# Performance work log

Hardware: AMD Instinct MI355X
Metric: run time of the kernel (lower is better)

## Reference

```python
import jax, jax.numpy as jnp
import numpy as np

ED = 1024   # encoder_dim
GH = 1024   # gnn_hidden
NL = 3      # gnn_layers
NH = 8      # gnn_heads
HD = GH // NH
N = 2048    # graph nodes
B = 1024    # query/doc batch
TEMP = 0.05
LAPW = 0.1

def _layernorm(x, g, b):
    mu = jnp.mean(x, axis=-1, keepdims=True)
    var = jnp.mean((x - mu) ** 2, axis=-1, keepdims=True)
    return (x - mu) * jax.lax.rsqrt(var + 1e-5) * g + b

def _mlp_proj(x, W1, b1, g, beta, W2, b2):
    h = _layernorm(x @ W1 + b1, g, beta)
    h = jax.nn.gelu(h, approximate=False)
    return h @ W2 + b2

def _l2norm(x):
    n = jnp.linalg.norm(x, axis=-1, keepdims=True)
    return x / jnp.maximum(n, 1e-12)

def _gnn(x, adj, gatW, a1, a2, ln_g, ln_b, poW, pob):
    mask = adj > 0
    for l in range(NL):
        Wh = jnp.einsum('nf,hfo->hno', x, gatW[l])            # [H,N,HD]
        # a([Wh_i, Wh_j]) == Wh_i@a1 + Wh_j@a2 (linear, no bias): avoids NxNx2F concat
        s1 = jnp.einsum('hno,ho->hn', Wh, a1[l])
        s2 = jnp.einsum('hno,ho->hn', Wh, a2[l])
        e = jax.nn.leaky_relu(s1[:, :, None] + s2[:, None, :], 0.2)  # [H,N,N]
        att = jax.nn.softmax(jnp.where(mask[None], e, -9e15), axis=-1)
        h = jnp.einsum('hnm,hmo->hno', att, Wh)               # [H,N,HD]
        h = jnp.transpose(h, (1, 0, 2)).reshape(x.shape[0], GH)  # concat heads
        h = jax.nn.elu(_layernorm(h, ln_g[l], ln_b[l]))
        x = x + h  # in_features == hidden so residual applies every layer
    return x @ poW + pob

def _forward(query_embeds, pos_doc_embeds, node_embeds, adj, laplacian, params):
    (qW1, qb1, qg, qbt, qW2, qb2,
     dW1, db1, dg, dbt, dW2, db2,
     gatW, a1, a2, ln_g, ln_b, poW, pob) = params
    graph_embeds = _gnn(node_embeds, adj, gatW, a1, a2, ln_g, ln_b, poW, pob)
    q = _l2norm(_mlp_proj(query_embeds, qW1, qb1, qg, qbt, qW2, qb2))
    p = _l2norm(_mlp_proj(pos_doc_embeds, dW1, db1, dg, dbt, dW2, db2))
    pos_sim = jnp.sum(q * p, axis=-1) / TEMP                  # [B]
    neg_sim = (q @ p.T) / TEMP                                # [B,B]
    logits = jnp.concatenate([pos_sim[:, None], neg_sim], axis=1)
    info_nce = jnp.mean(jax.nn.logsumexp(logits, axis=-1) - logits[:, 0])
    lap = jnp.sum(graph_embeds * (laplacian @ graph_embeds)) / graph_embeds.shape[0]
    return info_nce + LAPW * lap, info_nce, lap

def setup_inputs() -> dict:
    key = jax.random.key(0)
    ks = jax.random.split(key, 24)
    r = lambda k, s: jax.random.normal(k, s, jnp.float32) * 0.02
    adj = (jax.random.uniform(ks[3], (N, N)) < 0.02).astype(jnp.float32)
    adj = jnp.maximum(adj, jnp.eye(N, dtype=jnp.float32))
    return {
        'query_embeds': jax.random.normal(ks[0], (B, ED), jnp.float32),
        'pos_doc_embeds': jax.random.normal(ks[1], (B, ED), jnp.float32),
        'node_embeds': jax.random.normal(ks[2], (N, ED), jnp.float32),
        'adj': adj,
        'laplacian': r(ks[4], (N, N)),
        'qW1': r(ks[5], (ED, ED)), 'qb1': jnp.zeros((ED,), jnp.float32),
        'qg': jnp.ones((ED,), jnp.float32), 'qbt': jnp.zeros((ED,), jnp.float32),
        'qW2': r(ks[6], (ED, ED)), 'qb2': jnp.zeros((ED,), jnp.float32),
        'dW1': r(ks[7], (ED, ED)), 'db1': jnp.zeros((ED,), jnp.float32),
        'dg': jnp.ones((ED,), jnp.float32), 'dbt': jnp.zeros((ED,), jnp.float32),
        'dW2': r(ks[8], (ED, ED)), 'db2': jnp.zeros((ED,), jnp.float32),
        'gatW': r(ks[9], (NL, NH, ED, HD)),
        'a1': r(ks[10], (NL, NH, HD)),
        'a2': r(ks[11], (NL, NH, HD)),
        'ln_g': jnp.ones((NL, GH), jnp.float32),
        'ln_b': jnp.zeros((NL, GH), jnp.float32),
        'poW': r(ks[12], (GH, ED)),
        'pob': jnp.zeros((ED,), jnp.float32),
    }

def reference(query_embeds, pos_doc_embeds, node_embeds, adj, laplacian,
              qW1, qb1, qg, qbt, qW2, qb2,
              dW1, db1, dg, dbt, dW2, db2,
              gatW, a1, a2, ln_g, ln_b, poW, pob):
    params = (qW1, qb1, qg, qbt, qW2, qb2,
              dW1, db1, dg, dbt, dW2, db2,
              gatW, a1, a2, ln_g, ln_b, poW, pob)
    return _forward(query_embeds, pos_doc_embeds, node_embeds, adj, laplacian, params)
```

## Files before the change

### kernel.cpp

```cpp
#include <hip/hip_runtime.h>
#include <math.h>

#define ED    1024
#define GH    1024
#define NLAY  3
#define NHEAD 8
#define HD    128
#define NNODE 2048
#define BQ    1024
#define CAP   192
#define CAPP  208

typedef unsigned short u16;
typedef __attribute__((ext_vector_type(8))) short short8;
typedef __attribute__((ext_vector_type(4))) float f32x4;

static const size_t OFF_X    = 0;
static const size_t OFF_XB   = 2097152;
static const size_t OFF_WHB  = 3145728;
static const size_t OFF_WTG  = 4194304;
static const size_t OFF_WTPO = 5767168;
static const size_t OFF_WTQ1 = 6291456;
static const size_t OFF_WTD1 = 6815744;
static const size_t OFF_WTQ2 = 7340032;
static const size_t OFF_WTD2 = 7864320;
static const size_t OFF_G    = 8388608;
static const size_t OFF_GT   = 10485760;
static const size_t OFF_QPB  = 11534336;
static const size_t OFF_HF   = 12582912;
static const size_t OFF_HB   = 14680064;
static const size_t OFF_FF   = 15728640;
static const size_t OFF_FB   = 17825792;
static const size_t OFF_NEG  = 18874368;
static const size_t OFF_SV1  = 19922944;
static const size_t OFF_SV2  = 19939328;
static const size_t OFF_ACC  = 19955712;
static const size_t OFF_CNT  = 19955714;
static const size_t OFF_NCNT = 19955720;
static const size_t OFF_NBR  = 19957768;

__device__ __forceinline__ u16 f2bf(float f) {
  unsigned int u = __float_as_uint(f);
  return (u16)((u + 0x7fffu + ((u >> 16) & 1u)) >> 16);
}
__device__ __forceinline__ float bf2f(u16 u) {
  return __uint_as_float(((unsigned int)u) << 16);
}

__device__ __forceinline__ float waveSum(float v) {
#pragma unroll
  for (int off = 32; off; off >>= 1) v += __shfl_xor(v, off, 64);
  return v;
}
__device__ __forceinline__ float waveMax(float v) {
#pragma unroll
  for (int off = 32; off; off >>= 1) v = fmaxf(v, __shfl_xor(v, off, 64));
  return v;
}
__device__ __forceinline__ float blockSum(float v) {
  __shared__ float buf[4];
  int lane = threadIdx.x & 63, wid = threadIdx.x >> 6, nw = (blockDim.x + 63) >> 6;
  v = waveSum(v);
  __syncthreads();
  if (lane == 0) buf[wid] = v;
  __syncthreads();
  float r = buf[0];
  for (int i = 1; i < nw; ++i) r += buf[i];
  return r;
}
__device__ __forceinline__ float blockMax(float v) {
  __shared__ float buf[4];
  int lane = threadIdx.x & 63, wid = threadIdx.x >> 6, nw = (blockDim.x + 63) >> 6;
  v = waveMax(v);
  __syncthreads();
  if (lane == 0) buf[wid] = v;
  __syncthreads();
  float r = buf[0];
  for (int i = 1; i < nw; ++i) r = fmaxf(r, buf[i]);
  return r;
}

__global__ __launch_bounds__(256) void gemm128(
    const u16* __restrict__ A, const u16* __restrict__ B0,
    const u16* __restrict__ B1, float* __restrict__ C, u16* __restrict__ Cb,
    u16* __restrict__ Ct,
    const float* __restrict__ bias0, const float* __restrict__ bias1,
    int M, int N, int K, int split, float scale) {
  __shared__ u16 As[2][128][32];
  __shared__ u16 Bs[2][128][32];
  const int tid = threadIdx.x, wave = tid >> 6, lane = tid & 63;
  const int bm = blockIdx.y * 128, bn = blockIdx.x * 128;
  const u16* Bt = (bm < split) ? B0 : B1;
  const float* bias = (bm < split) ? bias0 : bias1;

  const int sr = tid >> 2, ss = tid & 3;
  const u16* ga0 = A  + (size_t)(bm + sr) * K + ss * 8;
  const u16* ga1 = A  + (size_t)(bm + sr + 64) * K + ss * 8;
  const u16* gb0 = Bt + (size_t)(bn + sr) * K + ss * 8;
  const u16* gb1 = Bt + (size_t)(bn + sr + 64) * K + ss * 8;

  const int r16 = lane & 15, kg = lane >> 4;
  const int wm = (wave >> 1) * 64, wn = (wave & 1) * 64;

  f32x4 acc[4][4] = {};
  const int nk = K >> 5;

  float4 pa0 = *(const float4*)ga0;
  float4 pa1 = *(const float4*)ga1;
  float4 pb0 = *(const float4*)gb0;
  float4 pb1 = *(const float4*)gb1;

  for (int kt = 0; kt < nk; ++kt) {
    const int p = kt & 1;
    *(float4*)&As[p][sr][ss * 8]      = pa0;
    *(float4*)&As[p][sr + 64][ss * 8] = pa1;
    *(float4*)&Bs[p][sr][ss * 8]      = pb0;
    *(float4*)&Bs[p][sr + 64][ss * 8] = pb1;
    __syncthreads();
    if (kt + 1 < nk) {
      ga0 += 32; ga1 += 32; gb0 += 32; gb1 += 32;
      pa0 = *(const float4*)ga0;
      pa1 = *(const float4*)ga1;
      pb0 = *(const float4*)gb0;
      pb1 = *(const float4*)gb1;
    }
    short8 av[4], bv[4];
#pragma unroll
    for (int i = 0; i < 4; ++i)
      av[i] = *(const short8*)&As[p][wm + i * 16 + r16][kg * 8];
#pragma unroll
    for (int j = 0; j < 4; ++j)
      bv[j] = *(const short8*)&Bs[p][wn + j * 16 + r16][kg * 8];
#pragma unroll
    for (int i = 0; i < 4; ++i)
#pragma unroll
      for (int j = 0; j < 4; ++j)
        acc[i][j] = __builtin_amdgcn_mfma_f32_16x16x32_bf16(av[i], bv[j], acc[i][j], 0, 0, 0);
  }

  if (C) {
#pragma unroll
    for (int j = 0; j < 4; ++j) {
      int col = bn + wn + j * 16 + r16;
      float bvv = bias ? bias[col] : 0.f;
#pragma unroll
      for (int i = 0; i < 4; ++i) {
        int row0 = bm + wm + i * 16 + kg * 4;
        float* cp = C + (size_t)row0 * N + col;
#pragma unroll
        for (int r = 0; r < 4; ++r)
          cp[(size_t)r * N] = acc[i][j][r] * scale + bvv;
      }
    }
  }
  if (Cb) {
#pragma unroll
    for (int j = 0; j < 4; ++j) {
      int col = bn + wn + j * 16 + r16;
      float bvv = bias ? bias[col] : 0.f;
#pragma unroll
      for (int i = 0; i < 4; ++i) {
        int row0 = bm + wm + i * 16 + kg * 4;
        u16* cp = Cb + (size_t)row0 * N + col;
#pragma unroll
        for (int r = 0; r < 4; ++r)
          cp[(size_t)r * N] = f2bf(acc[i][j][r] * scale + bvv);
      }
    }
  }
  if (Ct) {
#pragma unroll
    for (int j = 0; j < 4; ++j) {
      int col = bn + wn + j * 16 + r16;
      float bvv = bias ? bias[col] : 0.f;
#pragma unroll
      for (int i = 0; i < 4; ++i) {
        int row0 = bm + wm + i * 16 + kg * 4;
        ushort4 o;
        o.x = f2bf(acc[i][j][0] * scale + bvv);
        o.y = f2bf(acc[i][j][1] * scale + bvv);
        o.z = f2bf(acc[i][j][2] * scale + bvv);
        o.w = f2bf(acc[i][j][3] * scale + bvv);
        *(ushort4*)&Ct[(size_t)col * M + row0] = o;
      }
    }
  }
}

__global__ __launch_bounds__(256) void gemm_dual(
    const u16* __restrict__ A0, const u16* __restrict__ B00,
    const u16* __restrict__ B01, float* __restrict__ C0, u16* __restrict__ D0,
    const float* __restrict__ e0, const float* __restrict__ f0, int M0, int sp0, float sc0,
    const float* __restrict__ A1v, const float* __restrict__ A2v,
    float* __restrict__ S1o, float* __restrict__ S2o,
    const u16* __restrict__ A1, const u16* __restrict__ B10,
    const u16* __restrict__ B11, float* __restrict__ C1, u16* __restrict__ D1,
    const float* __restrict__ e1, const float* __restrict__ f1, int M1, int sp1, float sc1) {
  const int z = blockIdx.z;
  const u16* A   = z ? A1 : A0;
  const u16* Bt0 = z ? B10 : B00;
  const u16* Bt1 = z ? B11 : B01;
  float* C = z ? C1 : C0;
  u16*   D = z ? D1 : D0;
  const float* bias0 = z ? e1 : e0;
  const float* bias1 = z ? f1 : f0;
  const int M = z ? M1 : M0, split = z ? sp1 : sp0;
  const float scale = z ? sc1 : sc0;
  const int bm = blockIdx.y * 128, bn = blockIdx.x * 128;
  if (bm >= M) return;
  const int N = 1024, K = 1024;
  const u16* Bt = (bm < split) ? Bt0 : Bt1;
  const float* bias = (bm < split) ? bias0 : bias1;

  __shared__ u16 As[2][128][32];
  __shared__ u16 Bs[2][128][32];
  const int tid = threadIdx.x, wave = tid >> 6, lane = tid & 63;
  const int sr = tid >> 2, ss = tid & 3;
  const u16* ga0 = A  + (size_t)(bm + sr) * K + ss * 8;
  const u16* ga1 = A  + (size_t)(bm + sr + 64) * K + ss * 8;
  const u16* gb0 = Bt + (size_t)(bn + sr) * K + ss * 8;
  const u16* gb1 = Bt + (size_t)(bn + sr + 64) * K + ss * 8;
  const int r16 = lane & 15, kg = lane >> 4;
  const int wm = (wave >> 1) * 64, wn = (wave & 1) * 64;

  f32x4 acc[4][4] = {};
  const int nk = 32;

  float4 pa0 = *(const float4*)ga0;
  float4 pa1 = *(const float4*)ga1;
  float4 pb0 = *(const float4*)gb0;
  float4 pb1 = *(const float4*)gb1;

  for (int kt = 0; kt < nk; ++kt) {
    const int p = kt & 1;
    *(float4*)&As[p][sr][ss * 8]      = pa0;
    *(float4*)&As[p][sr + 64][ss * 8] = pa1;
    *(float4*)&Bs[p][sr][ss * 8]      = pb0;
    *(float4*)&Bs[p][sr + 64][ss * 8] = pb1;
    __syncthreads();
    if (kt + 1 < nk) {
      ga0 += 32; ga1 += 32; gb0 += 32; gb1 += 32;
      pa0 = *(const float4*)ga0;
      pa1 = *(const float4*)ga1;
      pb0 = *(const float4*)gb0;
      pb1 = *(const float4*)gb1;
    }
    short8 av[4], bv[4];
#pragma unroll
    for (int i = 0; i < 4; ++i)
      av[i] = *(const short8*)&As[p][wm + i * 16 + r16][kg * 8];
#pragma unroll
    for (int j = 0; j < 4; ++j)
      bv[j] = *(const short8*)&Bs[p][wn + j * 16 + r16][kg * 8];
#pragma unroll
    for (int i = 0; i < 4; ++i)
#pragma unroll
      for (int j = 0; j < 4; ++j)
        acc[i][j] = __builtin_amdgcn_mfma_f32_16x16x32_bf16(av[i], bv[j], acc[i][j], 0, 0, 0);
  }

  if (C) {
#pragma unroll
    for (int j = 0; j < 4; ++j) {
      int col = bn + wn + j * 16 + r16;
      float bvv = bias ? bias[col] : 0.f;
#pragma unroll
      for (int i = 0; i < 4; ++i) {
        int row0 = bm + wm + i * 16 + kg * 4;
        float* cp = C + (size_t)row0 * N + col;
#pragma unroll
        for (int r = 0; r < 4; ++r)
          cp[(size_t)r * N] = acc[i][j][r] * scale + bvv;
      }
    }
  }
  if (D) {
#pragma unroll
    for (int j = 0; j < 4; ++j) {
      int col = bn + wn + j * 16 + r16;
      float bvv = bias ? bias[col] : 0.f;
#pragma unroll
      for (int i = 0; i < 4; ++i) {
        int row0 = bm + wm + i * 16 + kg * 4;
        u16* cp = D + (size_t)row0 * N + col;
#pragma unroll
        for (int r = 0; r < 4; ++r)
          cp[(size_t)r * N] = f2bf(acc[i][j][r] * scale + bvv);
      }
    }
  }

  if (z == 0 && S1o) {
    float c1[4], c2[4];
#pragma unroll
    for (int j = 0; j < 4; ++j) {
      int col = bn + wn + j * 16 + r16;
      c1[j] = A1v[col]; c2[j] = A2v[col];
    }
    float r1[4][4], r2[4][4];
#pragma unroll
    for (int i = 0; i < 4; ++i)
#pragma unroll
      for (int r = 0; r < 4; ++r) {
        float v1 = 0.f, v2 = 0.f;
#pragma unroll
        for (int j = 0; j < 4; ++j) {
          v1 += acc[i][j][r] * c1[j];
          v2 += acc[i][j][r] * c2[j];
        }
#pragma unroll
        for (int off = 8; off; off >>= 1) {
          v1 += __shfl_xor(v1, off, 64);
          v2 += __shfl_xor(v2, off, 64);
        }
        r1[i][r] = v1; r2[i][r] = v2;
      }
    __syncthreads();
    float* sb1 = (float*)&As[0][0][0];
    float* sb2 = sb1 + 256;
    if (r16 == 0) {
      int half = wn >> 6;
#pragma unroll
      for (int i = 0; i < 4; ++i)
#pragma unroll
        for (int r = 0; r < 4; ++r) {
          int row = wm + i * 16 + kg * 4 + r;
          sb1[half * 128 + row] = r1[i][r];
          sb2[half * 128 + row] = r2[i][r];
        }
    }
    __syncthreads();
    if (tid < 128) {
      int h = blockIdx.x;
      S1o[(h << 11) + bm + tid] = sb1[tid] + sb1[128 + tid];
      S2o[(h << 11) + bm + tid] = sb2[tid] + sb2[128 + tid];
    }
  }
}

__global__ __launch_bounds__(256) void lap_gemm(
    const float* __restrict__ A, const u16* __restrict__ Bt,
    const float* __restrict__ G, float* __restrict__ acc,
    int* __restrict__ cnt_done, float* __restrict__ out) {
  __shared__ u16 As[2][128][32];
  __shared__ u16 Bs[2][128][32];
  const int tid = threadIdx.x, wave = tid >> 6, lane = tid & 63;
  const int n = blockIdx.x;
  const int bn = (n >> 7) * 128, strip = n & 127;
  const int bm = (strip & 15) * 128, k0 = (strip >> 4) * 256;

  const int sr = tid >> 2, ss = tid & 3;
  const float* gA0 = A + (size_t)(bm + sr) * NNODE + k0 + ss * 8;
  const float* gA1 = gA0 + (size_t)64 * NNODE;
  const u16* gb0 = Bt + (size_t)(bn + sr) * NNODE + k0 + ss * 8;
  const u16* gb1 = Bt + (size_t)(bn + sr + 64) * NNODE + k0 + ss * 8;

  const int r16 = lane & 15, kg = lane >> 4;
  const int wm = (wave >> 1) * 64, wn = (wave & 1) * 64;

  f32x4 acc_r[4][4] = {};
  const int nk = 8;

  float4 a0l = *(const float4*)gA0, a0h = *(const float4*)(gA0 + 4);
  float4 a1l = *(const float4*)gA1, a1h = *(const float4*)(gA1 + 4);
  float4 pb0 = *(const float4*)gb0;
  float4 pb1 = *(const float4*)gb1;

  for (int kt = 0; kt < nk; ++kt) {
    const int p = kt & 1;
    {
      union { short8 v; ushort4 u4[2]; } w;
      w.u4[0].x = f2bf(a0l.x); w.u4[0].y = f2bf(a0l.y);
      w.u4[0].z = f2bf(a0l.z); w.u4[0].w = f2bf(a0l.w);
      w.u4[1].x = f2bf(a0h.x); w.u4[1].y = f2bf(a0h.y);
      w.u4[1].z = f2bf(a0h.z); w.u4[1].w = f2bf(a0h.w);
      *(short8*)&As[p][sr][ss * 8] = w.v;
      w.u4[0].x = f2bf(a1l.x); w.u4[0].y = f2bf(a1l.y);
      w.u4[0].z = f2bf(a1l.z); w.u4[0].w = f2bf(a1l.w);
      w.u4[1].x = f2bf(a1h.x); w.u4[1].y = f2bf(a1h.y);
      w.u4[1].z = f2bf(a1h.z); w.u4[1].w = f2bf(a1h.w);
      *(short8*)&As[p][sr + 64][ss * 8] = w.v;
    }
    *(float4*)&Bs[p][sr][ss * 8]      = pb0;
    *(float4*)&Bs[p][sr + 64][ss * 8] = pb1;
    __syncthreads();
    if (kt + 1 < nk) {
      gA0 += 32; gA1 += 32; gb0 += 32; gb1 += 32;
      a0l = *(const float4*)gA0; a0h = *(const float4*)(gA0 + 4);
      a1l = *(const float4*)gA1; a1h = *(const float4*)(gA1 + 4);
      pb0 = *(const float4*)gb0;
      pb1 = *(const float4*)gb1;
    }
    short8 av[4], bv[4];
#pragma unroll
    for (int i = 0; i < 4; ++i)
      av[i] = *(const short8*)&As[p][wm + i * 16 + r16][kg * 8];
#pragma unroll
    for (int j = 0; j < 4; ++j)
      bv[j] = *(const short8*)&Bs[p][wn + j * 16 + r16][kg * 8];
#pragma unroll
    for (int i = 0; i < 4; ++i)
#pragma unroll
      for (int j = 0; j < 4; ++j)
        acc_r[i][j] = __builtin_amdgcn_mfma_f32_16x16x32_bf16(av[i], bv[j], acc_r[i][j], 0, 0, 0);
  }

  float sum = 0.f;
#pragma unroll
  for (int j = 0; j < 4; ++j) {
    int col = bn + wn + j * 16 + r16;
#pragma unroll
    for (int i = 0; i < 4; ++i) {
      int row0 = bm + wm + i * 16 + kg * 4;
      const float* gp = G + (size_t)row0 * ED + col;
#pragma unroll
      for (int r = 0; r < 4; ++r)
        sum += acc_r[i][j][r] * gp[(size_t)r * ED];
    }
  }
  sum = blockSum(sum);
  if (tid == 0) {
    atomicAdd(acc, sum);
    __threadfence();
    int prev = atomicAdd(cnt_done, 1);
    if (prev == (int)gridDim.x - 1) {
      float lap  = atomicAdd(acc, 0.f) / 2048.f;
      float info = atomicAdd(acc + 1, 0.f) / 1024.f;
      out[0] = info + 0.1f * lap;
      out[1] = info;
      out[2] = lap;
    }
  }
}

__global__ __launch_bounds__(256) void att_elem(
    const u16* __restrict__ WHb, const float* __restrict__ S1,
    const float* __restrict__ S2, const int* __restrict__ nbr,
    const int* __restrict__ ncnt, float* __restrict__ X, u16* __restrict__ Xb,
    const float* __restrict__ g, const float* __restrict__ b,
    int mode, const float* __restrict__ EIN, u16* __restrict__ EOUT,
    const float* __restrict__ g0, const float* __restrict__ b0,
    const float* __restrict__ g1, const float* __restrict__ b1,
    float* __restrict__ acc) {
  const int t = threadIdx.x;
  if (blockIdx.x < NNODE) {
    __shared__ int snb[CAPP];
    __shared__ float pw[NHEAD][CAPP];
    const int n = blockIdx.x;
    const int h = t >> 5, l = t & 31;
    const int cnt = ncnt[n];
    const int cntP = (cnt + 15) & ~15;
    for (int j = t; j < cnt; j += 256) snb[j] = nbr[n * CAP + j];
    __syncthreads();
    for (int j = cnt + t; j < cntP; j += 256) snb[j] = snb[0];

    const float s1v = S1[(h << 11) + n];
    float ev[6];
    float lmax = -1e30f;
    int ne = 0;
    for (int j = l; j < cnt; j += 32) {
      float e = s1v + S2[(h << 11) + snb[j]];
      e = e > 0.f ? e : 0.2f * e;
      ev[ne++] = e;
      lmax = fmaxf(lmax, e);
    }
#pragma unroll
    for (int off = 16; off; off >>= 1) lmax = fmaxf(lmax, __shfl_xor(lmax, off, 64));
    float lsum = 0.f;
    ne = 0;
    for (int j = l; j < cnt; j += 32) {
      float p = __expf(ev[ne++] - lmax);
      pw[h][j] = p;
      lsum += p;
    }
    for (int j = cnt + l; j < cntP; j += 32) pw[h][j] = 0.f;
#pragma unroll
    for (int off = 16; off; off >>= 1) lsum += __shfl_xor(lsum, off, 64);
    const float inv = 1.f / lsum;
    __syncthreads();

    float o0 = 0.f, o1 = 0.f, o2 = 0.f, o3 = 0.f;
    const u16* wp = WHb + (t << 2);
    for (int j0 = 0; j0 < cntP; j0 += 16) {
      ushort4 buf[16];
#pragma unroll
      for (int u = 0; u < 16; ++u)
        buf[u] = *(const ushort4*)(wp + ((size_t)snb[j0 + u] << 10));
#pragma unroll
      for (int u = 0; u < 16; ++u) {
        float w = pw[h][j0 + u];
        o0 += w * bf2f(buf[u].x);
        o1 += w * bf2f(buf[u].y);
        o2 += w * bf2f(buf[u].z);
        o3 += w * bf2f(buf[u].w);
      }
    }
    o0 *= inv; o1 *= inv; o2 *= inv; o3 *= inv;

    float s  = o0 + o1 + o2 + o3;
    float sq = o0 * o0 + o1 * o1 + o2 * o2 + o3 * o3;
    float mean = blockSum(s) * (1.f / 1024.f);
    float var  = blockSum(sq) * (1.f / 1024.f) - mean * mean;
    float rstd = rsqrtf(fmaxf(var, 0.f) + 1e-5f);
    float4 xv = *(float4*)&X[((size_t)n << 10) + (t << 2)];
    float ov[4] = {o0, o1, o2, o3};
    float xa[4] = {xv.x, xv.y, xv.z, xv.w};
#pragma unroll
    for (int i = 0; i < 4; ++i) {
      int c = (t << 2) + i;
      float y = (ov[i] - mean) * rstd * g[c] + b[c];
      y = y > 0.f ? y : expm1f(y);
      xa[i] += y;
    }
    *(float4*)&X[((size_t)n << 10) + (t << 2)] = make_float4(xa[0], xa[1], xa[2], xa[3]);
    ushort4 o;
    o.x = f2bf(xa[0]); o.y = f2bf(xa[1]); o.z = f2bf(xa[2]); o.w = f2bf(xa[3]);
    *(ushort4*)&Xb[((size_t)n << 10) + (t << 2)] = o;
  } else {
    const int row = blockIdx.x - NNODE;
    if (mode == 0) {
      const float* gg = (row < 1024) ? g0 : g1;
      const float* bb = (row < 1024) ? b0 : b1;
      float4 v = *(const float4*)&EIN[((size_t)row << 10) + (t << 2)];
      float s = v.x + v.y + v.z + v.w;
      float sq = v.x * v.x + v.y * v.y + v.z * v.z + v.w * v.w;
      float mean = blockSum(s) * (1.f / 1024.f);
      float var = blockSum(sq) * (1.f / 1024.f) - mean * mean;
      float rstd = rsqrtf(fmaxf(var, 0.f) + 1e-5f);
      float vals[4] = {v.x, v.y, v.z, v.w};
      ushort4 o;
      u16* oa = (u16*)&o;
#pragma unroll
      for (int i = 0; i < 4; ++i) {
        int c = (t << 2) + i;
        float y = (vals[i] - mean) * rstd * gg[c] + bb[c];
        y = 0.5f * y * (1.f + erff(y * 0.70710678118654752f));
        oa[i] = f2bf(y);
      }
      *(ushort4*)&EOUT[((size_t)row << 10) + (t << 2)] = o;
    } else if (mode == 1) {
      float4 v = *(const float4*)&EIN[((size_t)row << 10) + (t << 2)];
      float sq = v.x * v.x + v.y * v.y + v.z * v.z + v.w * v.w;
      float s = blockSum(sq);
      float inv = 1.f / fmaxf(sqrtf(s), 1e-12f);
      ushort4 o;
      o.x = f2bf(v.x * inv); o.y = f2bf(v.y * inv);
      o.z = f2bf(v.z * inv); o.w = f2bf(v.w * inv);
      *(ushort4*)&EOUT[((size_t)row << 10) + (t << 2)] = o;
    } else {
      const float* rw = EIN + ((size_t)row << 10);
      float4 v = *(const float4*)&rw[t << 2];
      float lm = fmaxf(fmaxf(v.x, v.y), fmaxf(v.z, v.w));
      float m = blockMax(lm);
      float ls = __expf(v.x - m) + __expf(v.y - m) + __expf(v.z - m) + __expf(v.w - m);
      float ssum = blockSum(ls);
      if (t == 0) {
        float pos = rw[row];
        float loss = m + logf(ssum + __expf(pos - m)) - pos;
        atomicAdd(acc + 1, loss);
      }
    }
  }
}

__global__ __launch_bounds__(256) void prep_mega(
    const float* __restrict__ adj, int* __restrict__ nbr, int* __restrict__ ncnt,
    float* __restrict__ acc, int* __restrict__ cnt_done,
    const float* __restrict__ nodes, float* __restrict__ Xf, u16* __restrict__ Xb,
    const float* __restrict__ q, const float* __restrict__ d, u16* __restrict__ QPb) {
  const int bx = blockIdx.x, tid = threadIdx.x;
  if (bx < NNODE) {
    __shared__ int cnt;
    if (bx == 0 && tid < 2) acc[tid] = 0.f;
    if (bx == 0 && tid == 2) *cnt_done = 0;
    if (tid == 0) cnt = 0;
    __syncthreads();
    for (int c = tid; c < NNODE; c += 256) {
      if (adj[((size_t)bx << 11) + c] > 0.f) {
        int p = atomicAdd(&cnt, 1);
        if (p < CAP) nbr[bx * CAP + p] = c;
      }
    }
    __syncthreads();
    if (tid == 0) ncnt[bx] = cnt < CAP ? cnt : CAP;
  } else if (bx < 2 * NNODE) {
    int i = (bx - NNODE) * 256 + tid;
    float4 v = ((const float4*)nodes)[i];
    ((float4*)Xf)[i] = v;
    ushort4 o;
    o.x = f2bf(v.x); o.y = f2bf(v.y); o.z = f2bf(v.z); o.w = f2bf(v.w);
    ((ushort4*)Xb)[i] = o;
  } else {
    int i = (bx - 2 * NNODE) * 256 + tid;
    const int half = BQ * ED / 4;
    const float* src = (i < half) ? q : d;
    int j = (i < half) ? i : i - half;
    float4 v = ((const float4*)src)[j];
    ushort4 o;
    o.x = f2bf(v.x); o.y = f2bf(v.y); o.z = f2bf(v.z); o.w = f2bf(v.w);
    ((ushort4*)QPb)[i] = o;
  }
}

__device__ __forceinline__ void cvt_tr_body(const float* ip, u16* op, int R, int C) {
  __shared__ float T[64][65];
  int r0 = blockIdx.y * 64, c0 = blockIdx.x * 64;
  int t = threadIdx.x;
#pragma unroll
  for (int p = 0; p < 4; ++p) {
    int row = p * 16 + (t >> 4), col = (t & 15) * 4;
    float4 v = *(const float4*)&ip[(size_t)(r0 + row) * C + c0 + col];
    T[row][col] = v.x; T[row][col + 1] = v.y;
    T[row][col + 2] = v.z; T[row][col + 3] = v.w;
  }
  __syncthreads();
#pragma unroll
  for (int p = 0; p < 4; ++p) {
    int c = p * 16 + (t >> 4), r = (t & 15) * 4;
    ushort4 o;
    o.x = f2bf(T[r][c]); o.y = f2bf(T[r + 1][c]);
    o.z = f2bf(T[r + 2][c]); o.w = f2bf(T[r + 3][c]);
    *(ushort4*)&op[(size_t)(c0 + c) * R + r0 + r] = o;
  }
}

__global__ __launch_bounds__(256) void cvt_transpose(
    const float* __restrict__ in, u16* __restrict__ out,
    int R, int C, long inb, long outb) {
  cvt_tr_body(in + (size_t)blockIdx.z * inb, out + (size_t)blockIdx.z * outb, R, C);
}

__global__ __launch_bounds__(256) void cvt_transpose5(
    const float* __restrict__ i0, u16* __restrict__ o0,
    const float* __restrict__ i1, u16* __restrict__ o1,
    const float* __restrict__ i2, u16* __restrict__ o2,
    const float* __restrict__ i3, u16* __restrict__ o3,
    const float* __restrict__ i4, u16* __restrict__ o4) {
  const float* in; u16* out;
  switch (blockIdx.z) {
    case 0: in = i0; out = o0; break;
    case 1: in = i1; out = o1; break;
    case 2: in = i2; out = o2; break;
    case 3: in = i3; out = o3; break;
    default: in = i4; out = o4; break;
  }
  cvt_tr_body(in, out, 1024, 1024);
}

extern "C" void kernel_launch(void* const* d_in, const int* in_sizes, int n_in,
                              void* d_out, int out_size, void* d_ws, size_t ws_size,
                              hipStream_t stream) {
  const float* query = (const float*)d_in[0];
  const float* docs  = (const float*)d_in[1];
  const float* nodes = (const float*)d_in[2];
  const float* adj   = (const float*)d_in[3];
  const float* lapl  = (const float*)d_in[4];
  const float* qW1 = (const float*)d_in[5],  *qb1 = (const float*)d_in[6];
  const float* qg  = (const float*)d_in[7],  *qbt = (const float*)d_in[8];
  const float* qW2 = (const float*)d_in[9],  *qb2 = (const float*)d_in[10];
  const float* dW1 = (const float*)d_in[11], *db1 = (const float*)d_in[12];
  const float* dg  = (const float*)d_in[13], *dbt = (const float*)d_in[14];
  const float* dW2 = (const float*)d_in[15], *db2 = (const float*)d_in[16];
  const float* gatW = (const float*)d_in[17];
  const float* a1   = (const float*)d_in[18];
  const float* a2   = (const float*)d_in[19];
  const float* ln_g = (const float*)d_in[20];
  const float* ln_b = (const float*)d_in[21];
  const float* poW  = (const float*)d_in[22];
  const float* pob  = (const float*)d_in[23];
  float* out = (float*)d_out;

  float* ws = (float*)d_ws;
  float* X    = ws + OFF_X;
  u16*   Xb   = (u16*)(ws + OFF_XB);
  u16*   WHb  = (u16*)(ws + OFF_WHB);
  u16*   WtG  = (u16*)(ws + OFF_WTG);
  u16*   WtPO = (u16*)(ws + OFF_WTPO);
  u16*   WtQ1 = (u16*)(ws + OFF_WTQ1);
  u16*   WtD1 = (u16*)(ws + OFF_WTD1);
  u16*   WtQ2 = (u16*)(ws + OFF_WTQ2);
  u16*   WtD2 = (u16*)(ws + OFF_WTD2);
  float* G    = ws + OFF_G;
  u16*   Gt   = (u16*)(ws + OFF_GT);
  u16*   QPb  = (u16*)(ws + OFF_QPB);
  float* Hf   = ws + OFF_HF;
  u16*   Hb   = (u16*)(ws + OFF_HB);
  float* Ff   = ws + OFF_FF;
  u16*   Fb   = (u16*)(ws + OFF_FB);
  float* NEG  = ws + OFF_NEG;
  float* S1v  = ws + OFF_SV1;
  float* S2v  = ws + OFF_SV2;
  float* ACC  = ws + OFF_ACC;
  int*   CNTD = (int*)(ws + OFF_CNT);
  int*   NCNT = (int*)(ws + OFF_NCNT);
  int*   NBR  = (int*)(ws + OFF_NBR);

  const size_t WSL = (size_t)GH * ED;

  prep_mega<<<3 * NNODE, 256, 0, stream>>>(
      adj, NBR, NCNT, ACC, CNTD, nodes, X, Xb, query, docs, QPb);
  cvt_transpose<<<dim3(2, 16, 24), 256, 0, stream>>>(
      gatW, WtG, ED, HD, (long)ED * HD, (long)HD * ED);
  cvt_transpose5<<<dim3(16, 16, 5), 256, 0, stream>>>(
      poW, WtPO, qW1, WtQ1, dW1, WtD1, qW2, WtQ2, dW2, WtD2);

  gemm_dual<<<dim3(8, 16, 2), 256, 0, stream>>>(
      Xb, WtG, WtG, nullptr, WHb, nullptr, nullptr, NNODE, NNODE, 1.f,
      a1, a2, S1v, S2v,
      QPb, WtQ1, WtD1, Hf, nullptr, qb1, db1, 2 * BQ, BQ, 1.f);
  att_elem<<<NNODE + 2 * BQ, 256, 0, stream>>>(
      WHb, S1v, S2v, NBR, NCNT, X, Xb, ln_g, ln_b,
      0, Hf, Hb, qg, qbt, dg, dbt, ACC);

  gemm_dual<<<dim3(8, 16, 2), 256, 0, stream>>>(
      Xb, WtG + WSL, WtG + WSL, nullptr, WHb, nullptr, nullptr, NNODE, NNODE, 1.f,
      a1 + NHEAD * HD, a2 + NHEAD * HD, S1v, S2v,
      Hb, WtQ2, WtD2, Ff, nullptr, qb2, db2, 2 * BQ, BQ, 1.f);
  att_elem<<<NNODE + 2 * BQ, 256, 0, stream>>>(
      WHb, S1v, S2v, NBR, NCNT, X, Xb, ln_g + GH, ln_b + GH,
      1, Ff, Fb, nullptr, nullptr, nullptr, nullptr, ACC);

  gemm_dual<<<dim3(8, 16, 2), 256, 0, stream>>>(
      Xb, WtG + 2 * WSL, WtG + 2 * WSL, nullptr, WHb, nullptr, nullptr, NNODE, NNODE, 1.f,
      a1 + 2 * NHEAD * HD, a2 + 2 * NHEAD * HD, S1v, S2v,
      Fb, Fb + (size_t)BQ * ED, Fb + (size_t)BQ * ED, NEG, nullptr,
      nullptr, nullptr, BQ, BQ, 20.f);
  att_elem<<<NNODE + BQ, 256, 0, stream>>>(
      WHb, S1v, S2v, NBR, NCNT, X, Xb, ln_g + 2 * GH, ln_b + 2 * GH,
      2, NEG, nullptr, nullptr, nullptr, nullptr, nullptr, ACC);

  gemm128<<<dim3(ED / 128, NNODE / 128), 256, 0, stream>>>(
      Xb, WtPO, WtPO, G, nullptr, Gt, pob, pob, NNODE, ED, GH, NNODE, 1.f);
  lap_gemm<<<1024, 256, 0, stream>>>(lapl, Gt, G, ACC, CNTD, out);
}
```

Baseline: 386.2 us.

## Compute Laplacian term as <L, G·Gᵀ> and swizzle LDS tiles in GEMMs

The Laplacian penalty sum(G * (L @ G)) is now computed as the Frobenius dot of L with G·Gᵀ. The new kernel forms 128x128 tiles of G·Gᵀ from bf16 G with K=1024 and dots them with fp32 L tiles, instead of streaming L through a K=2048 GEMM and reading G in fp32. This drops the fp32 G and transposed G outputs and the per-element fp32-to-bf16 conversion of L. All GEMM kernels also get an XOR swizzle on their shared-memory tile layout to reduce LDS bank conflicts. The grid shrinks from 1024 to 256 blocks, which may lower occupancy, and G now enters the result only in bf16.

```diff
diff --git a/kernel.cpp b/kernel.cpp
--- a/kernel.cpp
+++ b/kernel.cpp
@@ -24,8 +24,7 @@
 static const size_t OFF_WTD1 = 6815744;
 static const size_t OFF_WTQ2 = 7340032;
 static const size_t OFF_WTD2 = 7864320;
-static const size_t OFF_G    = 8388608;
-static const size_t OFF_GT   = 10485760;
+static const size_t OFF_GB   = 8388608;
 static const size_t OFF_QPB  = 11534336;
 static const size_t OFF_HF   = 12582912;
 static const size_t OFF_HB   = 14680064;
@@ -80,10 +79,11 @@
   return r;
 }
 
+#define SWZ(row, seg) (((seg) ^ (((row) >> 1) & 3)) << 3)
+
 __global__ __launch_bounds__(256) void gemm128(
     const u16* __restrict__ A, const u16* __restrict__ B0,
     const u16* __restrict__ B1, float* __restrict__ C, u16* __restrict__ Cb,
-    u16* __restrict__ Ct,
     const float* __restrict__ bias0, const float* __restrict__ bias1,
     int M, int N, int K, int split, float scale) {
   __shared__ u16 As[2][128][32];
@@ -94,6 +94,7 @@
   const float* bias = (bm < split) ? bias0 : bias1;
 
   const int sr = tid >> 2, ss = tid & 3;
+  const int so = SWZ(sr, ss);
   const u16* ga0 = A  + (size_t)(bm + sr) * K + ss * 8;
   const u16* ga1 = A  + (size_t)(bm + sr + 64) * K + ss * 8;
   const u16* gb0 = Bt + (size_t)(bn + sr) * K + ss * 8;
@@ -112,10 +113,10 @@
 
   for (int kt = 0; kt < nk; ++kt) {
     const int p = kt & 1;
-    *(float4*)&As[p][sr][ss * 8]      = pa0;
-    *(float4*)&As[p][sr + 64][ss * 8] = pa1;
-    *(float4*)&Bs[p][sr][ss * 8]      = pb0;
-    *(float4*)&Bs[p][sr + 64][ss * 8] = pb1;
+    *(float4*)&As[p][sr][so]      = pa0;
+    *(float4*)&As[p][sr + 64][so] = pa1;
+    *(float4*)&Bs[p][sr][so]      = pb0;
+    *(float4*)&Bs[p][sr + 64][so] = pb1;
     __syncthreads();
     if (kt + 1 < nk) {
       ga0 += 32; ga1 += 32; gb0 += 32; gb1 += 32;
@@ -126,11 +127,15 @@
     }
     short8 av[4], bv[4];
 #pragma unroll
-    for (int i = 0; i < 4; ++i)
-      av[i] = *(const short8*)&As[p][wm + i * 16 + r16][kg * 8];
-#pragma unroll
-    for (int j = 0; j < 4; ++j)
-      bv[j] = *(const short8*)&Bs[p][wn + j * 16 + r16][kg * 8];
+    for (int i = 0; i < 4; ++i) {
+      int row = wm + i * 16 + r16;
+      av[i] = *(const short8*)&As[p][row][SWZ(row, kg)];
+    }
+#pragma unroll
+    for (int j = 0; j < 4; ++j) {
+      int col = wn + j * 16 + r16;
+      bv[j] = *(const short8*)&Bs[p][col][SWZ(col, kg)];
+    }
 #pragma unroll
     for (int i = 0; i < 4; ++i)
 #pragma unroll
@@ -165,23 +170,6 @@
 #pragma unroll
         for (int r = 0; r < 4; ++r)
           cp[(size_t)r * N] = f2bf(acc[i][j][r] * scale + bvv);
-      }
-    }
-  }
-  if (Ct) {
-#pragma unroll
-    for (int j = 0; j < 4; ++j) {
-      int col = bn + wn + j * 16 + r16;
-      float bvv = bias ? bias[col] : 0.f;
-#pragma unroll
-      for (int i = 0; i < 4; ++i) {
-        int row0 = bm + wm + i * 16 + kg * 4;
-        ushort4 o;
-        o.x = f2bf(acc[i][j][0] * scale + bvv);
-        o.y = f2bf(acc[i][j][1] * scale + bvv);
-        o.z = f2bf(acc[i][j][2] * scale + bvv);
-        o.w = f2bf(acc[i][j][3] * scale + bvv);
-        *(ushort4*)&Ct[(size_t)col * M + row0] = o;
       }
     }
   }
@@ -216,6 +204,7 @@
   __shared__ u16 Bs[2][128][32];
   const int tid = threadIdx.x, wave = tid >> 6, lane = tid & 63;
   const int sr = tid >> 2, ss = tid & 3;
+  const int so = SWZ(sr, ss);
   const u16* ga0 = A  + (size_t)(bm + sr) * K + ss * 8;
   const u16* ga1 = A  + (size_t)(bm + sr + 64) * K + ss * 8;
   const u16* gb0 = Bt + (size_t)(bn + sr) * K + ss * 8;
@@ -233,10 +222,10 @@
 
   for (int kt = 0; kt < nk; ++kt) {
     const int p = kt & 1;
-    *(float4*)&As[p][sr][ss * 8]      = pa0;
-    *(float4*)&As[p][sr + 64][ss * 8] = pa1;
-    *(float4*)&Bs[p][sr][ss * 8]      = pb0;
-    *(float4*)&Bs[p][sr + 64][ss * 8] = pb1;
+    *(float4*)&As[p][sr][so]      = pa0;
+    *(float4*)&As[p][sr + 64][so] = pa1;
+    *(float4*)&Bs[p][sr][so]      = pb0;
+    *(float4*)&Bs[p][sr + 64][so] = pb1;
     __syncthreads();
     if (kt + 1 < nk) {
       ga0 += 32; ga1 += 32; gb0 += 32; gb1 += 32;
@@ -247,11 +236,15 @@
     }
     short8 av[4], bv[4];
 #pragma unroll
-    for (int i = 0; i < 4; ++i)
-      av[i] = *(const short8*)&As[p][wm + i * 16 + r16][kg * 8];
-#pragma unroll
-    for (int j = 0; j < 4; ++j)
-      bv[j] = *(const short8*)&Bs[p][wn + j * 16 + r16][kg * 8];
+    for (int i = 0; i < 4; ++i) {
+      int row = wm + i * 16 + r16;
+      av[i] = *(const short8*)&As[p][row][SWZ(row, kg)];
+    }
+#pragma unroll
+    for (int j = 0; j < 4; ++j) {
+      int col = wn + j * 16 + r16;
+      bv[j] = *(const short8*)&Bs[p][col][SWZ(col, kg)];
+    }
 #pragma unroll
     for (int i = 0; i < 4; ++i)
 #pragma unroll
@@ -338,66 +331,58 @@
   }
 }
 
-__global__ __launch_bounds__(256) void lap_gemm(
-    const float* __restrict__ A, const u16* __restrict__ Bt,
-    const float* __restrict__ G, float* __restrict__ acc,
-    int* __restrict__ cnt_done, float* __restrict__ out) {
+__global__ __launch_bounds__(256) void ggt_dot(
+    const u16* __restrict__ Gb, const float* __restrict__ L,
+    float* __restrict__ acc, int* __restrict__ cnt_done, float* __restrict__ out) {
   __shared__ u16 As[2][128][32];
   __shared__ u16 Bs[2][128][32];
   const int tid = threadIdx.x, wave = tid >> 6, lane = tid & 63;
-  const int n = blockIdx.x;
-  const int bn = (n >> 7) * 128, strip = n & 127;
-  const int bm = (strip & 15) * 128, k0 = (strip >> 4) * 256;
+  const int ti = blockIdx.x & 15, tj = blockIdx.x >> 4;
+  const int bm = ti * 128, bn = tj * 128;
 
   const int sr = tid >> 2, ss = tid & 3;
-  const float* gA0 = A + (size_t)(bm + sr) * NNODE + k0 + ss * 8;
-  const float* gA1 = gA0 + (size_t)64 * NNODE;
-  const u16* gb0 = Bt + (size_t)(bn + sr) * NNODE + k0 + ss * 8;
-  const u16* gb1 = Bt + (size_t)(bn + sr + 64) * NNODE + k0 + ss * 8;
+  const int so = SWZ(sr, ss);
+  const u16* ga0 = Gb + (size_t)(bm + sr) * ED + ss * 8;
+  const u16* ga1 = Gb + (size_t)(bm + sr + 64) * ED + ss * 8;
+  const u16* gb0 = Gb + (size_t)(bn + sr) * ED + ss * 8;
+  const u16* gb1 = Gb + (size_t)(bn + sr + 64) * ED + ss * 8;
 
   const int r16 = lane & 15, kg = lane >> 4;
   const int wm = (wave >> 1) * 64, wn = (wave & 1) * 64;
 
   f32x4 acc_r[4][4] = {};
-  const int nk = 8;
-
-  float4 a0l = *(const float4*)gA0, a0h = *(const float4*)(gA0 + 4);
-  float4 a1l = *(const float4*)gA1, a1h = *(const float4*)(gA1 + 4);
+  const int nk = 32;
+
+  float4 pa0 = *(const float4*)ga0;
+  float4 pa1 = *(const float4*)ga1;
   float4 pb0 = *(const float4*)gb0;
   float4 pb1 = *(const float4*)gb1;
 
   for (int kt = 0; kt < nk; ++kt) {
     const int p = kt & 1;
-    {
-      union { short8 v; ushort4 u4[2]; } w;
-      w.u4[0].x = f2bf(a0l.x); w.u4[0].y = f2bf(a0l.y);
-      w.u4[0].z = f2bf(a0l.z); w.u4[0].w = f2bf(a0l.w);
-      w.u4[1].x = f2bf(a0h.x); w.u4[1].y = f2bf(a0h.y);
-      w.u4[1].z = f2bf(a0h.z); w.u4[1].w = f2bf(a0h.w);
-      *(short8*)&As[p][sr][ss * 8] = w.v;
-      w.u4[0].x = f2bf(a1l.x); w.u4[0].y = f2bf(a1l.y);
-      w.u4[0].z = f2bf(a1l.z); w.u4[0].w = f2bf(a1l.w);
-      w.u4[1].x = f2bf(a1h.x); w.u4[1].y = f2bf(a1h.y);
-      w.u4[1].z = f2bf(a1h.z); w.u4[1].w = f2bf(a1h.w);
-      *(short8*)&As[p][sr + 64][ss * 8] = w.v;
-    }
-    *(float4*)&Bs[p][sr][ss * 8]      = pb0;
-    *(float4*)&Bs[p][sr + 64][ss * 8] = pb1;
+    *(float4*)&As[p][sr][so]      = pa0;
+    *(float4*)&As[p][sr + 64][so] = pa1;
+    *(float4*)&Bs[p][sr][so]      = pb0;
+    *(float4*)&Bs[p][sr + 64][so] = pb1;
     __syncthreads();
     if (kt + 1 < nk) {
-      gA0 += 32; gA1 += 32; gb0 += 32; gb1 += 32;
-      a0l = *(const float4*)gA0; a0h = *(const float4*)(gA0 + 4);
-      a1l = *(const float4*)gA1; a1h = *(const float4*)(gA1 + 4);
+      ga0 += 32; ga1 += 32; gb0 += 32; gb1 += 32;
+      pa0 = *(const float4*)ga0;
+      pa1 = *(const float4*)ga1;
       pb0 = *(const float4*)gb0;
       pb1 = *(const float4*)gb1;
     }
     short8 av[4], bv[4];
 #pragma unroll
-    for (int i = 0; i < 4; ++i)
-      av[i] = *(const short8*)&As[p][wm + i * 16 + r16][kg * 8];
-#pragma unroll
-    for (int j = 0; j < 4; ++j)
-      bv[j] = *(const short8*)&Bs[p][wn + j * 16 + r16][kg * 8];
+    for (int i = 0; i < 4; ++i) {
+      int row = wm + i * 16 + r16;
+      av[i] = *(const short8*)&As[p][row][SWZ(row, kg)];
+    }
+#pragma unroll
+    for (int j = 0; j < 4; ++j) {
+      int col = wn + j * 16 + r16;
+      bv[j] = *(const short8*)&Bs[p][col][SWZ(col, kg)];
+    }
 #pragma unroll
     for (int i = 0; i < 4; ++i)
 #pragma unroll
@@ -407,15 +392,14 @@
 
   float sum = 0.f;
 #pragma unroll
-  for (int j = 0; j < 4; ++j) {
-    int col = bn + wn + j * 16 + r16;
-#pragma unroll
-    for (int i = 0; i < 4; ++i) {
-      int row0 = bm + wm + i * 16 + kg * 4;
-      const float* gp = G + (size_t)row0 * ED + col;
-#pragma unroll
-      for (int r = 0; r < 4; ++r)
-        sum += acc_r[i][j][r] * gp[(size_t)r * ED];
+  for (int i = 0; i < 4; ++i) {
+#pragma unroll
+    for (int r = 0; r < 4; ++r) {
+      int ig = bm + wm + i * 16 + kg * 4 + r;
+      const float* lp = L + (size_t)ig * NNODE + bn + wn + r16;
+#pragma unroll
+      for (int j = 0; j < 4; ++j)
+        sum += acc_r[i][j][r] * lp[j * 16];
     }
   }
   sum = blockSum(sum);
@@ -680,8 +664,7 @@
   u16*   WtD1 = (u16*)(ws + OFF_WTD1);
   u16*   WtQ2 = (u16*)(ws + OFF_WTQ2);
   u16*   WtD2 = (u16*)(ws + OFF_WTD2);
-  float* G    = ws + OFF_G;
-  u16*   Gt   = (u16*)(ws + OFF_GT);
+  u16*   Gb   = (u16*)(ws + OFF_GB);
   u16*   QPb  = (u16*)(ws + OFF_QPB);
   float* Hf   = ws + OFF_HF;
   u16*   Hb   = (u16*)(ws + OFF_HB);
@@ -730,6 +713,6 @@
       2, NEG, nullptr, nullptr, nullptr, nullptr, nullptr, ACC);
 
   gemm128<<<dim3(ED / 128, NNODE / 128), 256, 0, stream>>>(
-      Xb, WtPO, WtPO, G, nullptr, Gt, pob, pob, NNODE, ED, GH, NNODE, 1.f);
-  lap_gemm<<<1024, 256, 0, stream>>>(lapl, Gt, G, ACC, CNTD, out);
-}
+      Xb, WtPO, WtPO, nullptr, Gb, pob, pob, NNODE, ED, GH, NNODE, 1.f);
+  ggt_dot<<<256, 256, 0, stream>>>(Gb, lapl, ACC, CNTD, out);
+}
```

Measured after the change: 372.6 us. -3.5%, faster.
